# Performance work log

Hardware: AMD Instinct MI355X
Metric: run time of the kernel (lower is better)

## Reference

```python
import jax, jax.numpy as jnp
import numpy as np

B, S, D, H, L, TPB = 4, 1020, 1024, 16, 4, 17
VOBS, VACT = 4096, 16
DH = D // H
EPS = 1e-3  # keras LayerNormalization default epsilon


def _ln(x, g, b):
    m = jnp.mean(x, axis=-1, keepdims=True)
    v = jnp.mean((x - m) ** 2, axis=-1, keepdims=True)
    return (x - m) * jax.lax.rsqrt(v + EPS) * g + b


def setup_inputs() -> dict:
    key = jax.random.key(0)
    ks = iter(jax.random.split(key, 64))
    def p(shape, s=0.02):
        return jax.random.normal(next(ks), shape, jnp.float32) * s
    pos = np.arange(S)
    is_obs = jnp.asarray((pos % TPB) < (TPB - 1))
    tok = jax.random.randint(next(ks), (B, S), 0, VOBS)
    tok = jnp.where(is_obs[None, :], tok, tok % VACT).astype(jnp.int32)
    d = dict(
        tokens=tok,
        pos_emb=p((S, D)), emb_obs=p((VOBS, D)), emb_act=p((VACT, D)),
        ln1_g=jnp.ones((L, D)), ln1_b=jnp.zeros((L, D)),
        wq=p((L, D, D)), bq=jnp.zeros((L, D)),
        wk=p((L, D, D)), bk=jnp.zeros((L, D)),
        wv=p((L, D, D)), bv=jnp.zeros((L, D)),
        wo=p((L, D, D)), bo=jnp.zeros((L, D)),
        ln2_g=jnp.ones((L, D)), ln2_b=jnp.zeros((L, D)),
        w1=p((L, D, 4 * D)), b1=jnp.zeros((L, 4 * D)),
        w2=p((L, 4 * D, D)), b2=jnp.zeros((L, D)),
        lnf_g=jnp.ones((D,)), lnf_b=jnp.zeros((D,)),
        ho1=p((D, D)), bo1=jnp.zeros((D,)),
        ho2=p((D, VOBS)), bo2=jnp.zeros((VOBS,)),
        he1=p((D, D)), be1=jnp.zeros((D,)),
        he2=p((D, 2)), be2=jnp.zeros((2,)),
    )
    return d


def reference(tokens, pos_emb, emb_obs, emb_act, ln1_g, ln1_b, wq, bq, wk, bk,
              wv, bv, wo, bo, ln2_g, ln2_b, w1, b1, w2, b2, lnf_g, lnf_b,
              ho1, bo1, ho2, bo2, he1, be1, he2, be2):
    pos = jnp.arange(S)
    is_obs = (pos % TPB) < (TPB - 1)  # obs positions within each block
    # token embedding: obs table on obs positions, act table on act positions
    x = jnp.where(is_obs[None, :, None],
                  emb_obs[jnp.minimum(tokens, VOBS - 1)],
                  emb_act[jnp.minimum(tokens, VACT - 1)])
    x = x + pos_emb[None]
    neg_mask = (1.0 - jnp.tril(jnp.ones((S, S), jnp.float32))) * -1e9
    inv_sqrt_dk = 1.0 / np.sqrt(DH).astype(np.float32)
    for i in range(L):
        h = _ln(x, ln1_g[i], ln1_b[i])
        q = (h @ wq[i] + bq[i]).reshape(B, S, H, DH).transpose(0, 2, 1, 3)
        k = (h @ wk[i] + bk[i]).reshape(B, S, H, DH).transpose(0, 2, 1, 3)
        v = (h @ wv[i] + bv[i]).reshape(B, S, H, DH).transpose(0, 2, 1, 3)
        scores = jnp.einsum('bhqd,bhkd->bhqk', q, k) * inv_sqrt_dk + neg_mask
        w = jax.nn.softmax(scores, axis=-1)
        o = jnp.einsum('bhqk,bhkd->bhqd', w, v).transpose(0, 2, 1, 3).reshape(B, S, D)
        x = x + (o @ wo[i] + bo[i])
        h = _ln(x, ln2_g[i], ln2_b[i])
        h = jax.nn.gelu(h @ w1[i] + b1[i], approximate=False) @ w2[i] + b2[i]
        x = x + h
    x = _ln(x, lnf_g, lnf_b)
    # head slices (static)
    p_np = np.arange(S)
    head_obs_idx = jnp.asarray(np.nonzero(((p_np + 1) % TPB) != (TPB - 1))[0])  # 960
    act_idx = jnp.asarray(np.nonzero((p_np % TPB) == (TPB - 1))[0])            # 60
    xo = x[:, head_obs_idx]
    logits_obs = jax.nn.relu(xo @ ho1 + bo1) @ ho2 + bo2   # [B, 960, VOBS]
    xe = x[:, act_idx]
    logits_ends = jax.nn.relu(xe @ he1 + be1) @ he2 + be2  # [B, 60, 2]
    return (logits_obs, logits_ends)
```

## Files before the change

### kernel.cpp

```cpp
#include <hip/hip_runtime.h>
#include <hip/hip_bf16.h>
#include <math.h>

namespace {

constexpr int kS = 1020, kD = 1024, kTPB = 17, kDH = 64;
constexpr int kVOBS = 4096, kVACT = 16;
constexpr int kBS = 4080;
constexpr float kEPS = 1e-3f;

typedef float f32x4 __attribute__((ext_vector_type(4)));
typedef __bf16 bfx8 __attribute__((ext_vector_type(8)));
typedef unsigned short u16;
typedef u16 us8 __attribute__((ext_vector_type(8)));
typedef u16 us4 __attribute__((ext_vector_type(4)));

__device__ __forceinline__ float bf2f(u16 u) {
  union { unsigned int i; float f; } v; v.i = (unsigned int)u << 16; return v.f;
}
__device__ __forceinline__ u16 f2bf(float f) {
  union { float f; unsigned int i; } v; v.f = f;
  unsigned int r = v.i + 0x7FFFu + ((v.i >> 16) & 1u);
  return (u16)(r >> 16);
}

__global__ void k_embed(const int* __restrict__ tokens, const float* __restrict__ pos_emb,
                        const float* __restrict__ emb_obs, const float* __restrict__ emb_act,
                        float* __restrict__ x) {
  int bs = blockIdx.x;
  int s = bs % kS;
  int tk = tokens[bs];
  bool obs = (s % kTPB) < (kTPB - 1);
  const float* e;
  if (obs) { int t2 = tk < kVOBS - 1 ? tk : kVOBS - 1; e = emb_obs + (size_t)t2 * kD; }
  else     { int t2 = tk < kVACT - 1 ? tk : kVACT - 1; e = emb_act + (size_t)t2 * kD; }
  int c = threadIdx.x * 4;
  float4 ev = *(const float4*)(e + c);
  float4 pv = *(const float4*)(pos_emb + (size_t)s * kD + c);
  float4 o; o.x = ev.x + pv.x; o.y = ev.y + pv.y; o.z = ev.z + pv.z; o.w = ev.w + pv.w;
  *(float4*)(x + (size_t)bs * kD + c) = o;
}

__global__ void k_pack_bias(const float* __restrict__ bq, const float* __restrict__ bk,
                            const float* __restrict__ bv, float* __restrict__ bqkv) {
  int idx = blockIdx.x * 256 + threadIdx.x;
  int l = idx / 3072, rem = idx % 3072;
  int sel = rem >> 10, cc = rem & 1023;
  const float* src = sel == 0 ? bq : (sel == 1 ? bk : bv);
  bqkv[idx] = src[l * kD + cc];
}

__global__ void k_ln(const float* __restrict__ x, const float* __restrict__ g,
                     const float* __restrict__ b, u16* __restrict__ out) {
  int row = blockIdx.x;
  int t = threadIdx.x;
  const float* xr = x + (size_t)row * kD;
  float4 v = *(const float4*)(xr + t * 4);
  float s1 = v.x + v.y + v.z + v.w;
  float s2 = v.x * v.x + v.y * v.y + v.z * v.z + v.w * v.w;
  #pragma unroll
  for (int m = 32; m; m >>= 1) { s1 += __shfl_xor(s1, m); s2 += __shfl_xor(s2, m); }
  __shared__ float ls1[4], ls2[4];
  int w = t >> 6;
  if ((t & 63) == 0) { ls1[w] = s1; ls2[w] = s2; }
  __syncthreads();
  float S1 = ls1[0] + ls1[1] + ls1[2] + ls1[3];
  float S2 = ls2[0] + ls2[1] + ls2[2] + ls2[3];
  float mean = S1 * (1.0f / kD);
  float var = S2 * (1.0f / kD) - mean * mean;
  float rs = rsqrtf(var + kEPS);
  int c = t * 4;
  float4 gv = *(const float4*)(g + c);
  float4 bv = *(const float4*)(b + c);
  us4 o;
  o[0] = f2bf((v.x - mean) * rs * gv.x + bv.x);
  o[1] = f2bf((v.y - mean) * rs * gv.y + bv.y);
  o[2] = f2bf((v.z - mean) * rs * gv.z + bv.z);
  o[3] = f2bf((v.w - mean) * rs * gv.w + bv.w);
  *(us4*)(out + (size_t)row * kD + c) = o;
}

__global__ void k_transpose(const float* __restrict__ in, u16* __restrict__ out,
                            int R, int C, int ld) {
  __shared__ float tile[32][33];
  int tx = threadIdx.x, ty = threadIdx.y;
  int c0 = blockIdx.x * 32, r0 = blockIdx.y * 32;
  #pragma unroll
  for (int i = 0; i < 4; ++i)
    tile[ty + i * 8][tx] = in[(size_t)(r0 + ty + i * 8) * ld + c0 + tx];
  __syncthreads();
  #pragma unroll
  for (int i = 0; i < 4; ++i)
    out[(size_t)(c0 + ty + i * 8) * R + r0 + tx] = f2bf(tile[tx][ty + i * 8]);
}

template <int EPI, int BM>
__global__ void __launch_bounds__(256)
k_gemm(const u16* __restrict__ A, const u16* __restrict__ Bt, const float* __restrict__ bias,
       const float* __restrict__ resid, void* __restrict__ out, int M, int N, int K, int ldo) {
  constexpr int MFRAG = BM / 32;
  __shared__ alignas(16) u16 As[BM][40];
  __shared__ alignas(16) u16 Bs[128][40];
  int tid = threadIdx.x;
  int m0 = blockIdx.x * BM, n0 = blockIdx.y * 128;
  int lane = tid & 63, wv = tid >> 6;
  int wm = wv >> 1, wn = wv & 1;
  f32x4 acc[MFRAG][4] = {};
  us8 zero8;
  #pragma unroll
  for (int z = 0; z < 8; ++z) zero8[z] = 0;
  int ko = (lane >> 4) * 8;

  for (int k0 = 0; k0 < K; k0 += 32) {
    #pragma unroll
    for (int it = 0; it < BM / 64; ++it) {
      int idx = it * 256 + tid;
      int r = idx >> 2;
      int c8 = (idx & 3) * 8;
      int gr = m0 + r;
      us8 va = (gr < M) ? *(const us8*)(A + (size_t)gr * K + k0 + c8) : zero8;
      *(us8*)(&As[r][c8]) = va;
    }
    #pragma unroll
    for (int it = 0; it < 2; ++it) {
      int idx = it * 256 + tid;
      int r = idx >> 2;
      int c8 = (idx & 3) * 8;
      us8 vb = *(const us8*)(Bt + (size_t)(n0 + r) * K + k0 + c8);
      *(us8*)(&Bs[r][c8]) = vb;
    }
    __syncthreads();
    bfx8 af[MFRAG], bfr[4];
    #pragma unroll
    for (int mf = 0; mf < MFRAG; ++mf)
      af[mf] = *(const bfx8*)(&As[wm * (BM / 2) + mf * 16 + (lane & 15)][ko]);
    #pragma unroll
    for (int nf = 0; nf < 4; ++nf)
      bfr[nf] = *(const bfx8*)(&Bs[wn * 64 + nf * 16 + (lane & 15)][ko]);
    #pragma unroll
    for (int mf = 0; mf < MFRAG; ++mf)
      #pragma unroll
      for (int nf = 0; nf < 4; ++nf)
        acc[mf][nf] = __builtin_amdgcn_mfma_f32_16x16x32_bf16(af[mf], bfr[nf], acc[mf][nf], 0, 0, 0);
    __syncthreads();
  }

  #pragma unroll
  for (int mf = 0; mf < MFRAG; ++mf) {
    #pragma unroll
    for (int nf = 0; nf < 4; ++nf) {
      int gcol = n0 + wn * 64 + nf * 16 + (lane & 15);
      float bv = bias ? bias[gcol] : 0.0f;
      #pragma unroll
      for (int r = 0; r < 4; ++r) {
        int grow = m0 + wm * (BM / 2) + mf * 16 + (lane >> 4) * 4 + r;
        if (grow >= M) continue;
        float val = acc[mf][nf][r] + bv;
        size_t off2 = (size_t)grow * ldo + gcol;
        if (EPI == 0) {
          ((u16*)out)[off2] = f2bf(val);
        } else if (EPI == 1) {
          ((u16*)out)[off2] = f2bf(val > 0.f ? val : 0.f);
        } else if (EPI == 2) {
          ((u16*)out)[off2] = f2bf(0.5f * val * (1.f + erff(val * 0.70710678118654752440f)));
        } else if (EPI == 3) {
          ((float*)out)[off2] = resid[off2] + val;
        } else {
          ((float*)out)[off2] = val;
        }
      }
    }
  }
}

__device__ __forceinline__ int swz(int row, int colu16) {
  return (row * 64 + colu16) ^ ((row & 7) << 3) ^ ((row & 24) << 1);
}

__global__ void __launch_bounds__(256)
k_attn(const u16* __restrict__ q, const u16* __restrict__ k, const u16* __restrict__ v,
       u16* __restrict__ o, int ldin) {
  __shared__ u16 Kl[64 * 64];
  __shared__ u16 Vt[64 * 64];
  const int qb = blockIdx.x * 64;
  const int bh = blockIdx.y;
  const int b = bh >> 4, hh = bh & 15;
  const int tid = threadIdx.x;
  const int lane = tid & 63, w = tid >> 6;
  const int g = lane >> 4, c = lane & 15;
  const int q0 = qb + w * 16;
  const size_t base = (size_t)(b * kS) * ldin + hh * kDH;

  bfx8 qf0, qf1;
  {
    int qr = q0 + c; if (qr >= kS) qr = kS - 1;
    const u16* qp = q + base + (size_t)qr * ldin + g * 8;
    qf0 = *(const bfx8*)(qp);
    qf1 = *(const bfx8*)(qp + 32);
  }

  float mst = -1e30f, lsum = 0.f;
  f32x4 ot[4] = {};

  const int ntiles = blockIdx.x + 1;
  for (int t = 0; t < ntiles; ++t) {
    const int kt = t * 64;
    {
      int kr = tid >> 2, ds2 = (tid & 3) * 16;
      int kg = kt + kr; if (kg >= kS) kg = kS - 1;
      const u16* kp = k + base + (size_t)kg * ldin + ds2;
      us8 a0 = *(const us8*)(kp);
      us8 a1 = *(const us8*)(kp + 8);
      *(us8*)(&Kl[swz(kr, ds2)]) = a0;
      *(us8*)(&Kl[swz(kr, ds2 + 8)]) = a1;
      const u16* vp = v + base + (size_t)kg * ldin + ds2;
      us8 b0 = *(const us8*)(vp);
      us8 b1 = *(const us8*)(vp + 8);
      #pragma unroll
      for (int i2 = 0; i2 < 8; ++i2) Vt[swz(ds2 + i2, kr)] = b0[i2];
      #pragma unroll
      for (int i2 = 0; i2 < 8; ++i2) Vt[swz(ds2 + 8 + i2, kr)] = b1[i2];
    }
    __syncthreads();

    f32x4 s[4];
    #pragma unroll
    for (int kb = 0; kb < 4; ++kb) {
      bfx8 kf0 = *(const bfx8*)(&Kl[swz(kb * 16 + c, g * 8)]);
      bfx8 kf1 = *(const bfx8*)(&Kl[swz(kb * 16 + c, g * 8 + 32)]);
      f32x4 acc = {};
      acc = __builtin_amdgcn_mfma_f32_16x16x32_bf16(kf0, qf0, acc, 0, 0, 0);
      acc = __builtin_amdgcn_mfma_f32_16x16x32_bf16(kf1, qf1, acc, 0, 0, 0);
      s[kb] = acc;
    }

    const int qg = q0 + c;
    const bool diag = (kt + 63 > q0);
    float p[4][4];
    float tmax = -1e30f;
    #pragma unroll
    for (int kb = 0; kb < 4; ++kb)
      #pragma unroll
      for (int r = 0; r < 4; ++r) {
        float val = s[kb][r] * 0.125f;
        if (diag && (kt + kb * 16 + g * 4 + r > qg)) val = -1e30f;
        p[kb][r] = val;
        tmax = fmaxf(tmax, val);
      }
    tmax = fmaxf(tmax, __shfl_xor(tmax, 16));
    tmax = fmaxf(tmax, __shfl_xor(tmax, 32));
    float mnew = fmaxf(mst, tmax);
    float alpha = __expf(mst - mnew);
    float psum = 0.f;
    #pragma unroll
    for (int kb = 0; kb < 4; ++kb)
      #pragma unroll
      for (int r = 0; r < 4; ++r) {
        float e = __expf(p[kb][r] - mnew);
        p[kb][r] = e;
        psum += e;
      }
    psum += __shfl_xor(psum, 16);
    psum += __shfl_xor(psum, 32);
    lsum = lsum * alpha + psum;
    mst = mnew;
    #pragma unroll
    for (int db = 0; db < 4; ++db) {
      ot[db][0] *= alpha; ot[db][1] *= alpha;
      ot[db][2] *= alpha; ot[db][3] *= alpha;
    }

    #pragma unroll
    for (int h = 0; h < 2; ++h) {
      bfx8 pf;
      #pragma unroll
      for (int j = 0; j < 8; ++j)
        pf[j] = (__bf16)p[2 * h + (j >> 2)][j & 3];
      #pragma unroll
      for (int db = 0; db < 4; ++db) {
        us4 lo = *(const us4*)(&Vt[swz(16 * db + c, 32 * h + 4 * g)]);
        us4 hi = *(const us4*)(&Vt[swz(16 * db + c, 32 * h + 16 + 4 * g)]);
        union { us8 u; bfx8 bf; } cv;
        cv.u[0] = lo[0]; cv.u[1] = lo[1]; cv.u[2] = lo[2]; cv.u[3] = lo[3];
        cv.u[4] = hi[0]; cv.u[5] = hi[1]; cv.u[6] = hi[2]; cv.u[7] = hi[3];
        ot[db] = __builtin_amdgcn_mfma_f32_16x16x32_bf16(cv.bf, pf, ot[db], 0, 0, 0);
      }
    }
    __syncthreads();
  }

  if (q0 + c < kS) {
    float inv = 1.0f / lsum;
    u16* op = o + (size_t)(b * kS) * kD + hh * kDH + (size_t)(q0 + c) * kD;
    #pragma unroll
    for (int db = 0; db < 4; ++db)
      #pragma unroll
      for (int r = 0; r < 4; ++r)
        op[16 * db + 4 * g + r] = f2bf(ot[db][r] * inv);
  }
}

__global__ void k_gather_obs(const u16* __restrict__ xf, u16* __restrict__ xo) {
  int r = blockIdx.x;
  int b = r / 960, rr = r % 960;
  int j = rr & 15, blk = rr >> 4;
  int s = blk * kTPB + j + (j == 15 ? 1 : 0);
  const unsigned int* src = (const unsigned int*)(xf + ((size_t)(b * kS + s)) * kD);
  unsigned int* dst = (unsigned int*)(xo + (size_t)r * kD);
  dst[threadIdx.x] = src[threadIdx.x];
  dst[threadIdx.x + 256] = src[threadIdx.x + 256];
}
__global__ void k_gather_act(const u16* __restrict__ xf, u16* __restrict__ xe) {
  int r = blockIdx.x;
  int b = r / 60, rr = r % 60;
  int s = rr * kTPB + (kTPB - 1);
  const unsigned int* src = (const unsigned int*)(xf + ((size_t)(b * kS + s)) * kD);
  unsigned int* dst = (unsigned int*)(xe + (size_t)r * kD);
  dst[threadIdx.x] = src[threadIdx.x];
  dst[threadIdx.x + 256] = src[threadIdx.x + 256];
}

__global__ void k_ends(const u16* __restrict__ t2, const float* __restrict__ he2,
                       const float* __restrict__ be2, float* __restrict__ out) {
  int r = blockIdx.x;
  int t = threadIdx.x;
  float p0 = 0.f, p1 = 0.f;
  for (int j = t; j < kD; j += 256) {
    float xv = bf2f(t2[(size_t)r * kD + j]);
    p0 += xv * he2[j * 2];
    p1 += xv * he2[j * 2 + 1];
  }
  #pragma unroll
  for (int msk = 32; msk; msk >>= 1) { p0 += __shfl_xor(p0, msk); p1 += __shfl_xor(p1, msk); }
  __shared__ float l0[4], l1[4];
  int w = t >> 6;
  if ((t & 63) == 0) { l0[w] = p0; l1[w] = p1; }
  __syncthreads();
  if (t == 0) {
    out[r * 2 + 0] = l0[0] + l0[1] + l0[2] + l0[3] + be2[0];
    out[r * 2 + 1] = l1[0] + l1[1] + l1[2] + l1[3] + be2[1];
  }
}

}

extern "C" void kernel_launch(void* const* d_in, const int* in_sizes, int n_in,
                              void* d_out, int out_size, void* d_ws, size_t ws_size,
                              hipStream_t stream) {
  const int*   tokens  = (const int*)  d_in[0];
  const float* pos_emb = (const float*)d_in[1];
  const float* emb_obs = (const float*)d_in[2];
  const float* emb_act = (const float*)d_in[3];
  const float* ln1_g = (const float*)d_in[4];
  const float* ln1_b = (const float*)d_in[5];
  const float* wq = (const float*)d_in[6];
  const float* bq = (const float*)d_in[7];
  const float* wk = (const float*)d_in[8];
  const float* bk = (const float*)d_in[9];
  const float* wv = (const float*)d_in[10];
  const float* bv = (const float*)d_in[11];
  const float* wo = (const float*)d_in[12];
  const float* bo = (const float*)d_in[13];
  const float* ln2_g = (const float*)d_in[14];
  const float* ln2_b = (const float*)d_in[15];
  const float* w1 = (const float*)d_in[16];
  const float* b1 = (const float*)d_in[17];
  const float* w2 = (const float*)d_in[18];
  const float* b2 = (const float*)d_in[19];
  const float* lnf_g = (const float*)d_in[20];
  const float* lnf_b = (const float*)d_in[21];
  const float* ho1 = (const float*)d_in[22];
  const float* bo1 = (const float*)d_in[23];
  const float* ho2 = (const float*)d_in[24];
  const float* bo2 = (const float*)d_in[25];
  const float* he1 = (const float*)d_in[26];
  const float* be1 = (const float*)d_in[27];
  const float* he2 = (const float*)d_in[28];
  const float* be2 = (const float*)d_in[29];
  (void)in_sizes; (void)n_in; (void)out_size; (void)ws_size;

  char* ws = (char*)d_ws;
  size_t off = 0;
  auto alloc = [&](size_t bytes) -> char* {
    char* p = ws + off; off += (bytes + 255) & ~(size_t)255; return p;
  };
  u16*   wTbig = (u16*)alloc((size_t)4096 * 1024 * 2);
  float* x  = (float*)alloc((size_t)kBS * kD * 4);
  u16*   h  = (u16*)alloc((size_t)kBS * kD * 2);
  char*  scr = alloc((size_t)kBS * 4096 * 2);
  float* bqkv = (float*)alloc((size_t)4 * 3072 * 4);
  const size_t slotB = (size_t)kBS * kD * 2;
  u16* qkv = (u16*)scr;
  u16* ob  = (u16*)(scr + (size_t)kBS * 3072 * 2);
  u16* mid = (u16*)scr;
  u16* xf = (u16*)scr;
  u16* xo = (u16*)(scr + slotB);
  u16* t1 = (u16*)(scr + 2 * slotB);
  u16* xe = (u16*)(scr + 3 * slotB);
  u16* t2 = (u16*)(scr + 3 * slotB + (size_t)240 * kD * 2 + 256);

  dim3 tb(32, 8);
  dim3 tg(32, 32);
  k_embed<<<kBS, 256, 0, stream>>>(tokens, pos_emb, emb_obs, emb_act, x);
  k_pack_bias<<<48, 256, 0, stream>>>(bq, bk, bv, bqkv);

  for (int i = 0; i < 4; ++i) {
    const size_t wOff = (size_t)i * kD * kD;
    k_ln<<<kBS, 256, 0, stream>>>(x, ln1_g + i * kD, ln1_b + i * kD, h);

    k_transpose<<<tg, tb, 0, stream>>>(wq + wOff, wTbig, 1024, 1024, 1024);
    k_transpose<<<tg, tb, 0, stream>>>(wk + wOff, wTbig + (size_t)1024 * 1024, 1024, 1024, 1024);
    k_transpose<<<tg, tb, 0, stream>>>(wv + wOff, wTbig + (size_t)2048 * 1024, 1024, 1024, 1024);
    k_gemm<0, 128><<<dim3(32, 24), 256, 0, stream>>>(h, wTbig, bqkv + i * 3072, nullptr, qkv,
                                                     kBS, 3072, 1024, 3072);

    k_attn<<<dim3(16, 64), 256, 0, stream>>>(qkv, qkv + 1024, qkv + 2048, ob, 3072);

    k_transpose<<<tg, tb, 0, stream>>>(wo + wOff, wTbig, 1024, 1024, 1024);
    k_gemm<3, 64><<<dim3(64, 8), 256, 0, stream>>>(ob, wTbig, bo + i * kD, x, x,
                                                   kBS, 1024, 1024, 1024);

    k_ln<<<kBS, 256, 0, stream>>>(x, ln2_g + i * kD, ln2_b + i * kD, h);

    for (int c = 0; c < 4; ++c)
      k_transpose<<<tg, tb, 0, stream>>>(w1 + (size_t)i * kD * 4096 + c * 1024,
                                         wTbig + (size_t)c * 1024 * 1024, 1024, 1024, 4096);
    k_gemm<2, 128><<<dim3(32, 32), 256, 0, stream>>>(h, wTbig, b1 + (size_t)i * 4096, nullptr,
                                                     mid, kBS, 4096, 1024, 4096);
    k_transpose<<<dim3(32, 128), tb, 0, stream>>>(w2 + (size_t)i * 4096 * kD, wTbig,
                                                  4096, 1024, 1024);
    k_gemm<3, 64><<<dim3(64, 8), 256, 0, stream>>>(mid, wTbig, b2 + i * kD, x, x,
                                                   kBS, 1024, 4096, 1024);
  }

  k_ln<<<kBS, 256, 0, stream>>>(x, lnf_g, lnf_b, xf);
  k_gather_obs<<<3840, 256, 0, stream>>>(xf, xo);
  k_gather_act<<<240, 256, 0, stream>>>(xf, xe);

  k_transpose<<<tg, tb, 0, stream>>>(ho1, wTbig, 1024, 1024, 1024);
  k_gemm<1, 64><<<dim3(60, 8), 256, 0, stream>>>(xo, wTbig, bo1, nullptr, t1,
                                                 3840, 1024, 1024, 1024);
  for (int c = 0; c < 4; ++c)
    k_transpose<<<tg, tb, 0, stream>>>(ho2 + c * 1024, wTbig + (size_t)c * 1024 * 1024,
                                       1024, 1024, 4096);
  k_gemm<4, 128><<<dim3(30, 32), 256, 0, stream>>>(t1, wTbig, bo2, nullptr,
                                                   (float*)d_out, 3840, 4096, 1024, 4096);
  k_transpose<<<tg, tb, 0, stream>>>(he1, wTbig, 1024, 1024, 1024);
  k_gemm<1, 64><<<dim3(4, 8), 256, 0, stream>>>(xe, wTbig, be1, nullptr, t2,
                                                240, 1024, 1024, 1024);
  k_ends<<<240, 256, 0, stream>>>(t2, he2, be2, (float*)d_out + (size_t)3840 * 4096);
}
```

Baseline: 1.526 ms.

## Load GEMM tiles directly to LDS with XOR swizzle and workgroup remap

Replaces the register-staged global-to-LDS copies in the GEMM with direct global_load_lds transfers into an unpadded LDS layout. Bank conflicts are avoided with an XOR swizzle of the 8-element chunks. Workgroup IDs are also remapped so that consecutive blocks are spread across column tiles, aiming for better cache locality across chiplets. Out-of-range A rows are clamped to the last row instead of zero-filled, and the swizzled remap assumes the workgroup count divides by 8.

```diff
diff --git a/kernel.cpp b/kernel.cpp
--- a/kernel.cpp
+++ b/kernel.cpp
@@ -99,44 +99,56 @@
 k_gemm(const u16* __restrict__ A, const u16* __restrict__ Bt, const float* __restrict__ bias,
        const float* __restrict__ resid, void* __restrict__ out, int M, int N, int K, int ldo) {
   constexpr int MFRAG = BM / 32;
-  __shared__ alignas(16) u16 As[BM][40];
-  __shared__ alignas(16) u16 Bs[128][40];
+  __shared__ alignas(16) u16 As[BM * 32];
+  __shared__ alignas(16) u16 Bs[128 * 32];
   int tid = threadIdx.x;
-  int m0 = blockIdx.x * BM, n0 = blockIdx.y * 128;
+  int nwg = gridDim.x * gridDim.y;
+  int lin = blockIdx.y * gridDim.x + blockIdx.x;
+  int swzid = (lin & 7) * (nwg >> 3) + (lin >> 3);
+  int m0 = (swzid % gridDim.x) * BM;
+  int n0 = (swzid / gridDim.x) * 128;
   int lane = tid & 63, wv = tid >> 6;
   int wm = wv >> 1, wn = wv & 1;
   f32x4 acc[MFRAG][4] = {};
-  us8 zero8;
-  #pragma unroll
-  for (int z = 0; z < 8; ++z) zero8[z] = 0;
-  int ko = (lane >> 4) * 8;
 
   for (int k0 = 0; k0 < K; k0 += 32) {
     #pragma unroll
-    for (int it = 0; it < BM / 64; ++it) {
-      int idx = it * 256 + tid;
-      int r = idx >> 2;
-      int c8 = (idx & 3) * 8;
-      int gr = m0 + r;
-      us8 va = (gr < M) ? *(const us8*)(A + (size_t)gr * K + k0 + c8) : zero8;
-      *(us8*)(&As[r][c8]) = va;
-    }
-    #pragma unroll
-    for (int it = 0; it < 2; ++it) {
-      int idx = it * 256 + tid;
-      int r = idx >> 2;
-      int c8 = (idx & 3) * 8;
-      us8 vb = *(const us8*)(Bt + (size_t)(n0 + r) * K + k0 + c8);
-      *(us8*)(&Bs[r][c8]) = vb;
+    for (int n = 0; n < BM / 64; ++n) {
+      int u = n * 256 + wv * 64 + lane;
+      int r = u >> 2, ch = u & 3;
+      int gr = m0 + r; if (gr >= M) gr = M - 1;
+      int cg = ch ^ ((r >> 1) & 3);
+      const u16* src = A + (size_t)gr * K + k0 + cg * 8;
+      __builtin_amdgcn_global_load_lds(
+          (const __attribute__((address_space(1))) unsigned int*)src,
+          (__attribute__((address_space(3))) unsigned int*)&As[(size_t)(n * 256 + wv * 64) * 8],
+          16, 0, 0);
+    }
+    #pragma unroll
+    for (int n = 0; n < 2; ++n) {
+      int u = n * 256 + wv * 64 + lane;
+      int r = u >> 2, ch = u & 3;
+      int cg = ch ^ ((r >> 1) & 3);
+      const u16* src = Bt + (size_t)(n0 + r) * K + k0 + cg * 8;
+      __builtin_amdgcn_global_load_lds(
+          (const __attribute__((address_space(1))) unsigned int*)src,
+          (__attribute__((address_space(3))) unsigned int*)&Bs[(size_t)(n * 256 + wv * 64) * 8],
+          16, 0, 0);
     }
     __syncthreads();
+
     bfx8 af[MFRAG], bfr[4];
-    #pragma unroll
-    for (int mf = 0; mf < MFRAG; ++mf)
-      af[mf] = *(const bfx8*)(&As[wm * (BM / 2) + mf * 16 + (lane & 15)][ko]);
-    #pragma unroll
-    for (int nf = 0; nf < 4; ++nf)
-      bfr[nf] = *(const bfx8*)(&Bs[wn * 64 + nf * 16 + (lane & 15)][ko]);
+    int ch = lane >> 4;
+    #pragma unroll
+    for (int mf = 0; mf < MFRAG; ++mf) {
+      int row = wm * (BM / 2) + mf * 16 + (lane & 15);
+      af[mf] = *(const bfx8*)(&As[row * 32 + ((ch ^ ((row >> 1) & 3)) << 3)]);
+    }
+    #pragma unroll
+    for (int nf = 0; nf < 4; ++nf) {
+      int row = wn * 64 + nf * 16 + (lane & 15);
+      bfr[nf] = *(const bfx8*)(&Bs[row * 32 + ((ch ^ ((row >> 1) & 3)) << 3)]);
+    }
     #pragma unroll
     for (int mf = 0; mf < MFRAG; ++mf)
       #pragma unroll
```

Result: faster. 1.458 ms (-4.4%).
